# Performance work log

Hardware: AMD Instinct MI355X
Metric: run time of the kernel (lower is better)

The kernel has to match this reference:

```python
import jax, jax.numpy as jnp
import numpy as np

N = 10000          # nodes
E = 80000          # edges
STATE_DIM = 18
HID = 1024
LAYERS = 4


def setup_inputs() -> dict:
    key = jax.random.key(0)
    ks = jax.random.split(key, 16)
    s = 0.02
    x = jax.random.normal(ks[0], (N, STATE_DIM), dtype=jnp.float32)
    edge_index = jax.random.randint(ks[1], (2, E), 0, N, dtype=jnp.int32)
    # frozen inverse-phase embedding projection (no bias)
    proj_w = jax.random.normal(ks[2], (STATE_DIM, HID), dtype=jnp.float32) * s
    # per-layer message MLP: Linear(2*HID -> HID) -> ReLU -> Linear(HID -> HID)
    W1 = jax.random.normal(ks[3], (LAYERS, 2 * HID, HID), dtype=jnp.float32) * s
    b1 = jnp.zeros((LAYERS, HID), dtype=jnp.float32)
    W2 = jax.random.normal(ks[4], (LAYERS, HID, HID), dtype=jnp.float32) * s
    b2 = jnp.zeros((LAYERS, HID), dtype=jnp.float32)
    # ghost head: Linear(HID->256) -> ReLU -> Linear(256->1) -> Sigmoid
    gw1 = jax.random.normal(ks[5], (HID, 256), dtype=jnp.float32) * s
    gb1 = jnp.zeros((256,), dtype=jnp.float32)
    gw2 = jax.random.normal(ks[6], (256, 1), dtype=jnp.float32) * s
    gb2 = jnp.zeros((1,), dtype=jnp.float32)
    # state head: Linear(HID -> STATE_DIM)
    sw = jax.random.normal(ks[7], (HID, STATE_DIM), dtype=jnp.float32) * s
    sb = jnp.zeros((STATE_DIM,), dtype=jnp.float32)
    return {"x": x, "edge_index": edge_index, "proj_w": proj_w,
            "W1": W1, "b1": b1, "W2": W2, "b2": b2,
            "gw1": gw1, "gb1": gb1, "gw2": gw2, "gb2": gb2,
            "sw": sw, "sb": sb}


def reference(x, edge_index, proj_w, W1, b1, W2, b2, gw1, gb1, gw2, gb2, sw, sb):
    src = edge_index[0]  # j (source)
    dst = edge_index[1]  # i (target), aggr='add' scatters into i
    # InversePhaseEmbedding: sin(h)*cos(h)
    p = x @ proj_w                      # [N, HID]
    h = jnp.sin(p) * jnp.cos(p)
    for l in range(LAYERS):
        x_i = h[dst]                    # [E, HID] gather target feats
        x_j = h[src]                    # [E, HID] gather source feats
        msg = jnp.concatenate([x_i, x_j - x_i], axis=-1)  # [E, 2*HID]
        m = jax.nn.relu(msg @ W1[l] + b1[l]) @ W2[l] + b2[l]  # [E, HID]
        h = jax.ops.segment_sum(m, dst, num_segments=N)       # scatter-add
        h = jax.nn.relu(h)
    ghost_score = jax.nn.sigmoid(jax.nn.relu(h @ gw1 + gb1) @ gw2 + gb2)  # [N,1]
    stable_state = h @ sw + sb                                            # [N,18]
    return ghost_score, stable_state, h
```

## Files before the change

kernel.cpp:

```cpp
#include <hip/hip_runtime.h>
#include <hip/hip_bf16.h>
#include <math.h>

#define NN 10000
#define EE 80000
#define SDIM 18
#define HID 1024
#define NLAYERS 4
#define GHID 256

typedef __bf16 bf16;
typedef __bf16 bf16x8 __attribute__((ext_vector_type(8)));
typedef __bf16 bf16x4 __attribute__((ext_vector_type(4)));
typedef float f32x4 __attribute__((ext_vector_type(4)));

#define AS1C(p) ((const __attribute__((address_space(1))) void*)(p))
#define AS3(p)  ((__attribute__((address_space(3))) void*)(p))

__global__ void zeroi_kernel(int* __restrict__ p, int n) {
    int i = blockIdx.x * 256 + threadIdx.x;
    if (i < n) p[i] = 0;
}

__global__ void count_kernel(const int* __restrict__ ei, int* __restrict__ cnt) {
    int e = blockIdx.x * 256 + threadIdx.x;
    if (e < EE) atomicAdd(&cnt[ei[EE + e]], 1);
}

__global__ __launch_bounds__(256) void scan_kernel(const int* __restrict__ cnt,
                                                   int* __restrict__ offs,
                                                   int* __restrict__ cursor,
                                                   float* __restrict__ degF) {
    const int CH = 40;
    __shared__ int partial[256];
    int t = threadIdx.x;
    int base = t * CH;
    int local[CH];
    int sum = 0;
#pragma unroll
    for (int i = 0; i < CH; ++i) {
        int idx = base + i;
        int v = (idx < NN) ? cnt[idx] : 0;
        local[i] = sum;
        sum += v;
    }
    partial[t] = sum;
    __syncthreads();
    for (int off = 1; off < 256; off <<= 1) {
        int v = (t >= off) ? partial[t - off] : 0;
        __syncthreads();
        partial[t] += v;
        __syncthreads();
    }
    int excl = (t == 0) ? 0 : partial[t - 1];
#pragma unroll
    for (int i = 0; i < CH; ++i) {
        int idx = base + i;
        if (idx < NN) {
            int o = excl + local[i];
            offs[idx] = o;
            cursor[idx] = o;
            degF[idx] = (float)cnt[idx];
        }
    }
    if (t == 255) offs[NN] = partial[255];
}

__global__ void scatter_kernel(const int* __restrict__ ei, int* __restrict__ cursor,
                               int* __restrict__ esrc) {
    int e = blockIdx.x * 256 + threadIdx.x;
    if (e < EE) {
        int dst = ei[EE + e];
        int pos = atomicAdd(&cursor[dst], 1);
        esrc[pos] = ei[e];
    }
}

__global__ __launch_bounds__(256) void tconvW1_kernel(const float* __restrict__ W1,
                                                      bf16* __restrict__ WT) {
    __shared__ float td[32][33];
    __shared__ float tb[32][33];
    const size_t H2 = (size_t)HID * HID;
    const float* s = W1 + (size_t)blockIdx.z * 2 * H2;
    bf16* d = WT + (size_t)blockIdx.z * 2 * H2;
    int bx = blockIdx.x * 32;
    int by = blockIdx.y * 32;
    int tx = threadIdx.x, ty = threadIdx.y;
#pragma unroll
    for (int r = 0; r < 4; ++r) {
        int row = by + ty + r * 8;
        float vt = s[(size_t)row * HID + bx + tx];
        float vb = s[H2 + (size_t)row * HID + bx + tx];
        td[ty + r * 8][tx] = vt - vb;
        tb[ty + r * 8][tx] = vb;
    }
    __syncthreads();
#pragma unroll
    for (int r = 0; r < 4; ++r) {
        int orow = bx + ty + r * 8;
        d[(size_t)orow * HID + by + tx] = (bf16)td[tx][ty + r * 8];
        d[(size_t)(HID + orow) * HID + by + tx] = (bf16)tb[tx][ty + r * 8];
    }
}

__global__ __launch_bounds__(256) void tconv_kernel(const float* __restrict__ src, long sstride,
                                                    bf16* __restrict__ dst, long dstride,
                                                    int M, int N) {
    __shared__ float t[32][33];
    const float* s = src + (size_t)blockIdx.z * sstride;
    bf16* d = dst + (size_t)blockIdx.z * dstride;
    int bx = blockIdx.x * 32;
    int by = blockIdx.y * 32;
    int tx = threadIdx.x, ty = threadIdx.y;
#pragma unroll
    for (int r = 0; r < 4; ++r) {
        int row = by + ty + r * 8;
        t[ty + r * 8][tx] = s[(size_t)row * N + bx + tx];
    }
    __syncthreads();
#pragma unroll
    for (int r = 0; r < 4; ++r) {
        int orow = bx + ty + r * 8;
        d[(size_t)orow * M + by + tx] = (bf16)t[tx][ty + r * 8];
    }
}

__global__ void swt_kernel(const float* __restrict__ sw, bf16* __restrict__ swt) {
    int i = blockIdx.x * 256 + threadIdx.x;
    int n = i >> 10, k = i & 1023;
    swt[i] = (bf16)(n < SDIM ? sw[k * SDIM + n] : 0.f);
}

__global__ void bias2_kernel(const float* __restrict__ b1, float* __restrict__ cb) {
    int i = blockIdx.x * 256 + threadIdx.x;
    int l = i >> 11, c = i & 2047;
    cb[i] = (c < HID) ? b1[l * HID + c] : 0.f;
}

__global__ __launch_bounds__(256) void proj_kernel(const float* __restrict__ x,
                                                   const float* __restrict__ pw,
                                                   bf16* __restrict__ hb) {
    int row = blockIdx.y;
    int col = blockIdx.x * 256 + threadIdx.x;
    __shared__ float xr[SDIM];
    if (threadIdx.x < SDIM) xr[threadIdx.x] = x[row * SDIM + threadIdx.x];
    __syncthreads();
    float acc = 0.f;
#pragma unroll
    for (int k = 0; k < SDIM; ++k) acc += xr[k] * pw[k * HID + col];
    hb[(size_t)row * HID + col] = (bf16)(sinf(acc) * cosf(acc));
}

template <int RELU, int HAS_BIAS, int HAS_RS, int WF32, int WB16>
__global__ __launch_bounds__(256) void mgemm_kernel(const bf16* __restrict__ A,
                                                    const bf16* __restrict__ Bt,
                                                    float* __restrict__ C,
                                                    bf16* __restrict__ Cb,
                                                    const float* __restrict__ bias,
                                                    const float* __restrict__ rowscale,
                                                    int M, int N, int K) {
    __shared__ bf16 As[2 * 128 * 32];
    __shared__ bf16 Bs[2 * 128 * 32];
    const int tid = threadIdx.x;

    const int num_n = gridDim.x, num_m = gridDim.y;
    int bid = blockIdx.x + blockIdx.y * num_n;
    const int GROUP = 8;
    int width = GROUP * num_n;
    int group = bid / width;
    int rem = bid - group * width;
    int rows_ing = num_m - group * GROUP;
    rows_ing = rows_ing < GROUP ? rows_ing : GROUP;
    int by = group * GROUP + rem % rows_ing;
    int bx = rem / rows_ing;
    const int m0 = by * 128;
    const int n0 = bx * 128;

    const int wave = tid >> 6;
    const int wr = (wave >> 1) * 64, wc = (wave & 1) * 64;
    const int lane = tid & 63;
    const int quad = lane >> 4, r15 = lane & 15;

    f32x4 acc[4][4] = {};

    const int s0 = tid, s1 = 256 + tid;
    int ar0 = m0 + (s0 >> 2); ar0 = ar0 < M ? ar0 : M - 1;
    int ar1 = m0 + (s1 >> 2); ar1 = ar1 < M ? ar1 : M - 1;
    const bf16* ga0 = A + (size_t)ar0 * K + (s0 & 3) * 8;
    const bf16* ga1 = A + (size_t)ar1 * K + (s1 & 3) * 8;
    const bf16* gb0 = Bt + (size_t)(n0 + (s0 >> 2)) * K + (s0 & 3) * 8;
    const bf16* gb1 = Bt + (size_t)(n0 + (s1 >> 2)) * K + (s1 & 3) * 8;
    bf16* lA0 = As + (size_t)(tid & ~63) * 8;
    bf16* lA1 = As + (size_t)(256 + (tid & ~63)) * 8;
    bf16* lB0 = Bs + (size_t)(tid & ~63) * 8;
    bf16* lB1 = Bs + (size_t)(256 + (tid & ~63)) * 8;

    for (int k0 = 0; k0 < K; k0 += 64) {
        __syncthreads();
        __builtin_amdgcn_global_load_lds(AS1C(ga0 + k0), AS3(lA0), 16, 0, 0);
        __builtin_amdgcn_global_load_lds(AS1C(ga1 + k0), AS3(lA1), 16, 0, 0);
        __builtin_amdgcn_global_load_lds(AS1C(ga0 + k0 + 32), AS3(lA0 + 4096), 16, 0, 0);
        __builtin_amdgcn_global_load_lds(AS1C(ga1 + k0 + 32), AS3(lA1 + 4096), 16, 0, 0);
        __builtin_amdgcn_global_load_lds(AS1C(gb0 + k0), AS3(lB0), 16, 0, 0);
        __builtin_amdgcn_global_load_lds(AS1C(gb1 + k0), AS3(lB1), 16, 0, 0);
        __builtin_amdgcn_global_load_lds(AS1C(gb0 + k0 + 32), AS3(lB0 + 4096), 16, 0, 0);
        __builtin_amdgcn_global_load_lds(AS1C(gb1 + k0 + 32), AS3(lB1 + 4096), 16, 0, 0);
        __syncthreads();
#pragma unroll
        for (int hf = 0; hf < 2; ++hf) {
            bf16x8 af[4], bfr[4];
#pragma unroll
            for (int i = 0; i < 4; ++i)
                af[i] = *(const bf16x8*)(As + hf * 4096 + (wr + i * 16 + r15) * 32 + quad * 8);
#pragma unroll
            for (int j = 0; j < 4; ++j)
                bfr[j] = *(const bf16x8*)(Bs + hf * 4096 + (wc + j * 16 + r15) * 32 + quad * 8);
#pragma unroll
            for (int i = 0; i < 4; ++i)
#pragma unroll
                for (int j = 0; j < 4; ++j)
                    acc[i][j] = __builtin_amdgcn_mfma_f32_16x16x32_bf16(af[i], bfr[j], acc[i][j], 0, 0, 0);
        }
    }

#pragma unroll
    for (int i = 0; i < 4; ++i) {
#pragma unroll
        for (int r = 0; r < 4; ++r) {
            int grow = m0 + wr + i * 16 + quad * 4 + r;
            if (grow >= M) continue;
            float rs = HAS_RS ? rowscale[grow] : 1.f;
#pragma unroll
            for (int j = 0; j < 4; ++j) {
                int gcol = n0 + wc + j * 16 + r15;
                float v = acc[i][j][r];
                if (HAS_BIAS) v += rs * bias[gcol];
                if (RELU) v = fmaxf(v, 0.f);
                if (WF32) C[(size_t)grow * N + gcol] = v;
                if (WB16) Cb[(size_t)grow * N + gcol] = (bf16)v;
            }
        }
    }
}

__global__ __launch_bounds__(256) void gather_kernel(const int* __restrict__ offs,
                                                     const int* __restrict__ esrc,
                                                     const bf16* __restrict__ CB,
                                                     bf16* __restrict__ Sb) {
    int node = blockIdx.x;
    int c = threadIdx.x * 4;
    int k0 = offs[node], k1 = offs[node + 1];
    bf16x4 cv = *(const bf16x4*)(CB + (size_t)node * 2048 + c);
    float cx = (float)cv.x, cy = (float)cv.y, cz = (float)cv.z, cw = (float)cv.w;
    float ax = 0.f, ay = 0.f, az = 0.f, aw = 0.f;
    for (int k = k0; k < k1; ++k) {
        int s = esrc[k];
        bf16x4 bv = *(const bf16x4*)(CB + (size_t)s * 2048 + 1024 + c);
        ax += fmaxf(cx + (float)bv.x, 0.f);
        ay += fmaxf(cy + (float)bv.y, 0.f);
        az += fmaxf(cz + (float)bv.z, 0.f);
        aw += fmaxf(cw + (float)bv.w, 0.f);
    }
    bf16x4 o;
    o.x = (bf16)ax; o.y = (bf16)ay; o.z = (bf16)az; o.w = (bf16)aw;
    *(bf16x4*)(Sb + (size_t)node * HID + c) = o;
}

__global__ __launch_bounds__(64) void stable_mfma_kernel(const bf16* __restrict__ hb,
                                                         const bf16* __restrict__ swt,
                                                         const float* __restrict__ sb,
                                                         float* __restrict__ out) {
    int m0 = blockIdx.x * 16;
    int lane = threadIdx.x;
    int quad = lane >> 4, r15 = lane & 15;
    f32x4 acc0 = {}, acc1 = {};
    const bf16* arow = hb + (size_t)(m0 + r15) * HID + quad * 8;
    const bf16* b0 = swt + (size_t)r15 * HID + quad * 8;
    const bf16* b1p = swt + (size_t)(16 + r15) * HID + quad * 8;
    for (int k0 = 0; k0 < HID; k0 += 32) {
        bf16x8 af = *(const bf16x8*)(arow + k0);
        bf16x8 bf0 = *(const bf16x8*)(b0 + k0);
        bf16x8 bf1 = *(const bf16x8*)(b1p + k0);
        acc0 = __builtin_amdgcn_mfma_f32_16x16x32_bf16(af, bf0, acc0, 0, 0, 0);
        acc1 = __builtin_amdgcn_mfma_f32_16x16x32_bf16(af, bf1, acc1, 0, 0, 0);
    }
#pragma unroll
    for (int r = 0; r < 4; ++r) {
        int grow = m0 + quad * 4 + r;
        out[(size_t)grow * SDIM + r15] = acc0[r] + sb[r15];
        if (r15 < 2) out[(size_t)grow * SDIM + 16 + r15] = acc1[r] + sb[16 + r15];
    }
}

__global__ __launch_bounds__(256) void ghost_kernel(const float* __restrict__ g1,
                                                    const float* __restrict__ gw2,
                                                    const float* __restrict__ gb2,
                                                    float* __restrict__ out) {
    int row = blockIdx.x;
    int t = threadIdx.x;
    float v = g1[(size_t)row * GHID + t] * gw2[t];
#pragma unroll
    for (int o = 32; o > 0; o >>= 1) v += __shfl_down(v, o, 64);
    __shared__ float red[4];
    if ((t & 63) == 0) red[t >> 6] = v;
    __syncthreads();
    if (t == 0) {
        float s = red[0] + red[1] + red[2] + red[3] + gb2[0];
        out[row] = 1.f / (1.f + expf(-s));
    }
}

extern "C" void kernel_launch(void* const* d_in, const int* in_sizes, int n_in,
                              void* d_out, int out_size, void* d_ws, size_t ws_size,
                              hipStream_t stream) {
    const float* x   = (const float*)d_in[0];
    const int*   ei  = (const int*)d_in[1];
    const float* pw  = (const float*)d_in[2];
    const float* W1  = (const float*)d_in[3];
    const float* b1  = (const float*)d_in[4];
    const float* W2  = (const float*)d_in[5];
    const float* b2  = (const float*)d_in[6];
    const float* gw1 = (const float*)d_in[7];
    const float* gb1 = (const float*)d_in[8];
    const float* gw2 = (const float*)d_in[9];
    const float* gb2 = (const float*)d_in[10];
    const float* sw  = (const float*)d_in[11];
    const float* sb  = (const float*)d_in[12];

    float* out    = (float*)d_out;
    float* ghost  = out;
    float* stable = out + NN;
    float* h      = out + NN + NN * SDIM;

    const size_t H2 = (size_t)HID * HID;
    float* ws   = (float*)d_ws;
    float* g1   = ws;
    float* degF = g1 + (size_t)NN * GHID;
    float* cb   = degF + NN;
    bf16* hb    = (bf16*)(cb + 4 * 2048);
    bf16* Sb    = hb + (size_t)NN * HID;
    bf16* CB    = Sb + (size_t)NN * HID;
    bf16* WT    = CB + (size_t)NN * 2048;
    bf16* W2t   = WT + 8 * H2;
    bf16* gw1t  = W2t + 4 * H2;
    bf16* swt   = gw1t + (size_t)GHID * HID;
    int*  cnt    = (int*)(swt + 32 * 1024);
    int*  offs   = cnt + NN;
    int*  cursor = offs + NN + 1;
    int*  esrc   = cursor + NN;

    zeroi_kernel<<<dim3((NN + 255) / 256), 256, 0, stream>>>(cnt, NN);
    count_kernel<<<dim3((EE + 255) / 256), 256, 0, stream>>>(ei, cnt);
    scan_kernel<<<dim3(1), 256, 0, stream>>>(cnt, offs, cursor, degF);
    scatter_kernel<<<dim3((EE + 255) / 256), 256, 0, stream>>>(ei, cursor, esrc);

    dim3 tb(32, 8);
    tconvW1_kernel<<<dim3(32, 32, 4), tb, 0, stream>>>(W1, WT);
    tconv_kernel<<<dim3(32, 32, 4), tb, 0, stream>>>(W2, (long)H2, W2t, (long)H2, HID, HID);
    tconv_kernel<<<dim3(GHID / 32, HID / 32, 1), tb, 0, stream>>>(gw1, 0, gw1t, 0, HID, GHID);
    swt_kernel<<<dim3(32 * 1024 / 256), 256, 0, stream>>>(sw, swt);
    bias2_kernel<<<dim3(4 * 2048 / 256), 256, 0, stream>>>(b1, cb);

    proj_kernel<<<dim3(HID / 256, NN), 256, 0, stream>>>(x, pw, hb);

    dim3 gfused(2048 / 128, (NN + 127) / 128);
    dim3 gw2g(HID / 128, (NN + 127) / 128);
    for (int l = 0; l < NLAYERS; ++l) {
        mgemm_kernel<0, 1, 0, 0, 1><<<gfused, 256, 0, stream>>>(
            hb, WT + (size_t)l * 2 * H2, nullptr, CB, cb + l * 2048, nullptr, NN, 2048, HID);
        gather_kernel<<<dim3(NN), 256, 0, stream>>>(offs, esrc, CB, Sb);
        if (l < NLAYERS - 1)
            mgemm_kernel<1, 1, 1, 0, 1><<<gw2g, 256, 0, stream>>>(
                Sb, W2t + (size_t)l * H2, nullptr, hb, b2 + (size_t)l * HID, degF, NN, HID, HID);
        else
            mgemm_kernel<1, 1, 1, 1, 1><<<gw2g, 256, 0, stream>>>(
                Sb, W2t + (size_t)l * H2, h, hb, b2 + (size_t)l * HID, degF, NN, HID, HID);
    }

    mgemm_kernel<1, 1, 0, 1, 0><<<dim3(GHID / 128, (NN + 127) / 128), 256, 0, stream>>>(
        hb, gw1t, g1, nullptr, gb1, nullptr, NN, GHID, HID);
    ghost_kernel<<<dim3(NN), 256, 0, stream>>>(g1, gw2, gb2, ghost);
    stable_mfma_kernel<<<dim3(NN / 16), 64, 0, stream>>>(hb, swt, sb, stable);
}
```

Baseline: 777.3 us.

## Double-buffer GEMM LDS loads, merge prep kernels, widen gather and ghost kernels

The GEMM main loop now uses two LDS buffers with K-step 32, so the next tile is prefetched while MFMAs run on the current one. The earlier version loaded a 64-wide K slice under two barriers with no overlap. All weight transpose, bias and zeroing kernels are merged into one prep launch to cut launch overhead. The gather kernel handles two nodes per block with 8-wide bf16 vectors, and the ghost head uses one wave per row without shared-memory reduction. Risks are twice as many barriers per K and more LDS pressure in the GEMM.

Measured after the change: 750.8 us. 3.4% less time.

```diff
diff --git a/kernel.cpp b/kernel.cpp
--- a/kernel.cpp
+++ b/kernel.cpp
@@ -16,11 +16,6 @@
 
 #define AS1C(p) ((const __attribute__((address_space(1))) void*)(p))
 #define AS3(p)  ((__attribute__((address_space(3))) void*)(p))
-
-__global__ void zeroi_kernel(int* __restrict__ p, int n) {
-    int i = blockIdx.x * 256 + threadIdx.x;
-    if (i < n) p[i] = 0;
-}
 
 __global__ void count_kernel(const int* __restrict__ ei, int* __restrict__ cnt) {
     int e = blockIdx.x * 256 + threadIdx.x;
@@ -76,65 +71,86 @@
     }
 }
 
-__global__ __launch_bounds__(256) void tconvW1_kernel(const float* __restrict__ W1,
-                                                      bf16* __restrict__ WT) {
+__global__ __launch_bounds__(256) void prep_kernel(const float* __restrict__ W1,
+                                                   const float* __restrict__ W2,
+                                                   const float* __restrict__ gw1,
+                                                   const float* __restrict__ sw,
+                                                   const float* __restrict__ b1,
+                                                   bf16* __restrict__ WT,
+                                                   bf16* __restrict__ W2t,
+                                                   bf16* __restrict__ gw1t,
+                                                   bf16* __restrict__ swt,
+                                                   float* __restrict__ cb,
+                                                   int* __restrict__ cnt) {
     __shared__ float td[32][33];
     __shared__ float tb[32][33];
     const size_t H2 = (size_t)HID * HID;
-    const float* s = W1 + (size_t)blockIdx.z * 2 * H2;
-    bf16* d = WT + (size_t)blockIdx.z * 2 * H2;
-    int bx = blockIdx.x * 32;
-    int by = blockIdx.y * 32;
-    int tx = threadIdx.x, ty = threadIdx.y;
-#pragma unroll
-    for (int r = 0; r < 4; ++r) {
-        int row = by + ty + r * 8;
-        float vt = s[(size_t)row * HID + bx + tx];
-        float vb = s[H2 + (size_t)row * HID + bx + tx];
-        td[ty + r * 8][tx] = vt - vb;
-        tb[ty + r * 8][tx] = vb;
-    }
-    __syncthreads();
-#pragma unroll
-    for (int r = 0; r < 4; ++r) {
-        int orow = bx + ty + r * 8;
-        d[(size_t)orow * HID + by + tx] = (bf16)td[tx][ty + r * 8];
-        d[(size_t)(HID + orow) * HID + by + tx] = (bf16)tb[tx][ty + r * 8];
-    }
-}
-
-__global__ __launch_bounds__(256) void tconv_kernel(const float* __restrict__ src, long sstride,
-                                                    bf16* __restrict__ dst, long dstride,
-                                                    int M, int N) {
-    __shared__ float t[32][33];
-    const float* s = src + (size_t)blockIdx.z * sstride;
-    bf16* d = dst + (size_t)blockIdx.z * dstride;
-    int bx = blockIdx.x * 32;
-    int by = blockIdx.y * 32;
-    int tx = threadIdx.x, ty = threadIdx.y;
-#pragma unroll
-    for (int r = 0; r < 4; ++r) {
-        int row = by + ty + r * 8;
-        t[ty + r * 8][tx] = s[(size_t)row * N + bx + tx];
-    }
-    __syncthreads();
-#pragma unroll
-    for (int r = 0; r < 4; ++r) {
-        int orow = bx + ty + r * 8;
-        d[(size_t)orow * M + by + tx] = (bf16)t[tx][ty + r * 8];
-    }
-}
-
-__global__ void swt_kernel(const float* __restrict__ sw, bf16* __restrict__ swt) {
-    int i = blockIdx.x * 256 + threadIdx.x;
-    int n = i >> 10, k = i & 1023;
-    swt[i] = (bf16)(n < SDIM ? sw[k * SDIM + n] : 0.f);
-}
-
-__global__ void bias2_kernel(const float* __restrict__ b1, float* __restrict__ cb) {
-    int i = blockIdx.x * 256 + threadIdx.x;
-    int l = i >> 11, c = i & 2047;
-    cb[i] = (c < HID) ? b1[l * HID + c] : 0.f;
+    int b = blockIdx.x;
+    int tx = threadIdx.x & 31, ty = threadIdx.x >> 5;
+
+    if (b < 4096) {
+        int l = b >> 10, r = b & 1023;
+        int bx = (r & 31) * 32, by = (r >> 5) * 32;
+        const float* s = W1 + (size_t)l * 2 * H2;
+        bf16* d = WT + (size_t)l * 2 * H2;
+#pragma unroll
+        for (int r4 = 0; r4 < 4; ++r4) {
+            int row = by + ty + r4 * 8;
+            float vt = s[(size_t)row * HID + bx + tx];
+            float vb = s[H2 + (size_t)row * HID + bx + tx];
+            td[ty + r4 * 8][tx] = vt - vb;
+            tb[ty + r4 * 8][tx] = vb;
+        }
+        __syncthreads();
+#pragma unroll
+        for (int r4 = 0; r4 < 4; ++r4) {
+            int orow = bx + ty + r4 * 8;
+            d[(size_t)orow * HID + by + tx] = (bf16)td[tx][ty + r4 * 8];
+            d[(size_t)(HID + orow) * HID + by + tx] = (bf16)tb[tx][ty + r4 * 8];
+        }
+    } else if (b < 8192) {
+        int sub = b - 4096;
+        int l = sub >> 10, r = sub & 1023;
+        int bx = (r & 31) * 32, by = (r >> 5) * 32;
+        const float* s = W2 + (size_t)l * H2;
+        bf16* d = W2t + (size_t)l * H2;
+#pragma unroll
+        for (int r4 = 0; r4 < 4; ++r4) {
+            int row = by + ty + r4 * 8;
+            td[ty + r4 * 8][tx] = s[(size_t)row * HID + bx + tx];
+        }
+        __syncthreads();
+#pragma unroll
+        for (int r4 = 0; r4 < 4; ++r4) {
+            int orow = bx + ty + r4 * 8;
+            d[(size_t)orow * HID + by + tx] = (bf16)td[tx][ty + r4 * 8];
+        }
+    } else if (b < 8448) {
+        int sub = b - 8192;
+        int bx = (sub & 7) * 32, by = (sub >> 3) * 32;
+#pragma unroll
+        for (int r4 = 0; r4 < 4; ++r4) {
+            int row = by + ty + r4 * 8;
+            td[ty + r4 * 8][tx] = gw1[(size_t)row * GHID + bx + tx];
+        }
+        __syncthreads();
+#pragma unroll
+        for (int r4 = 0; r4 < 4; ++r4) {
+            int orow = bx + ty + r4 * 8;
+            gw1t[(size_t)orow * HID + by + tx] = (bf16)td[tx][ty + r4 * 8];
+        }
+    } else if (b < 8576) {
+        int i = (b - 8448) * 256 + threadIdx.x;
+        int n = i >> 10, k = i & 1023;
+        swt[i] = (bf16)(n < SDIM ? sw[k * SDIM + n] : 0.f);
+    } else if (b < 8608) {
+        int i = (b - 8576) * 256 + threadIdx.x;
+        int l = i >> 11, c = i & 2047;
+        cb[i] = (c < HID) ? b1[l * HID + c] : 0.f;
+    } else {
+        int i = (b - 8608) * 256 + threadIdx.x;
+        if (i < NN) cnt[i] = 0;
+    }
 }
 
 __global__ __launch_bounds__(256) void proj_kernel(const float* __restrict__ x,
@@ -159,8 +175,8 @@
                                                     const float* __restrict__ bias,
                                                     const float* __restrict__ rowscale,
                                                     int M, int N, int K) {
-    __shared__ bf16 As[2 * 128 * 32];
-    __shared__ bf16 Bs[2 * 128 * 32];
+    __shared__ bf16 As[2][128 * 32];
+    __shared__ bf16 Bs[2][128 * 32];
     const int tid = threadIdx.x;
 
     const int num_n = gridDim.x, num_m = gridDim.y;
@@ -190,37 +206,37 @@
     const bf16* ga1 = A + (size_t)ar1 * K + (s1 & 3) * 8;
     const bf16* gb0 = Bt + (size_t)(n0 + (s0 >> 2)) * K + (s0 & 3) * 8;
     const bf16* gb1 = Bt + (size_t)(n0 + (s1 >> 2)) * K + (s1 & 3) * 8;
-    bf16* lA0 = As + (size_t)(tid & ~63) * 8;
-    bf16* lA1 = As + (size_t)(256 + (tid & ~63)) * 8;
-    bf16* lB0 = Bs + (size_t)(tid & ~63) * 8;
-    bf16* lB1 = Bs + (size_t)(256 + (tid & ~63)) * 8;
-
-    for (int k0 = 0; k0 < K; k0 += 64) {
-        __syncthreads();
-        __builtin_amdgcn_global_load_lds(AS1C(ga0 + k0), AS3(lA0), 16, 0, 0);
-        __builtin_amdgcn_global_load_lds(AS1C(ga1 + k0), AS3(lA1), 16, 0, 0);
-        __builtin_amdgcn_global_load_lds(AS1C(ga0 + k0 + 32), AS3(lA0 + 4096), 16, 0, 0);
-        __builtin_amdgcn_global_load_lds(AS1C(ga1 + k0 + 32), AS3(lA1 + 4096), 16, 0, 0);
-        __builtin_amdgcn_global_load_lds(AS1C(gb0 + k0), AS3(lB0), 16, 0, 0);
-        __builtin_amdgcn_global_load_lds(AS1C(gb1 + k0), AS3(lB1), 16, 0, 0);
-        __builtin_amdgcn_global_load_lds(AS1C(gb0 + k0 + 32), AS3(lB0 + 4096), 16, 0, 0);
-        __builtin_amdgcn_global_load_lds(AS1C(gb1 + k0 + 32), AS3(lB1 + 4096), 16, 0, 0);
-        __syncthreads();
-#pragma unroll
-        for (int hf = 0; hf < 2; ++hf) {
-            bf16x8 af[4], bfr[4];
-#pragma unroll
-            for (int i = 0; i < 4; ++i)
-                af[i] = *(const bf16x8*)(As + hf * 4096 + (wr + i * 16 + r15) * 32 + quad * 8);
+    const int lofs0 = (tid & ~63) * 8;
+    const int lofs1 = 2048 + (tid & ~63) * 8;
+
+    __builtin_amdgcn_global_load_lds(AS1C(ga0), AS3(&As[0][lofs0]), 16, 0, 0);
+    __builtin_amdgcn_global_load_lds(AS1C(ga1), AS3(&As[0][lofs1]), 16, 0, 0);
+    __builtin_amdgcn_global_load_lds(AS1C(gb0), AS3(&Bs[0][lofs0]), 16, 0, 0);
+    __builtin_amdgcn_global_load_lds(AS1C(gb1), AS3(&Bs[0][lofs1]), 16, 0, 0);
+
+    const int NIT = K >> 5;
+    for (int k = 0; k < NIT; ++k) {
+        const int buf = k & 1;
+        __syncthreads();
+        if (k + 1 < NIT) {
+            const int ko = (k + 1) << 5;
+            __builtin_amdgcn_global_load_lds(AS1C(ga0 + ko), AS3(&As[buf ^ 1][lofs0]), 16, 0, 0);
+            __builtin_amdgcn_global_load_lds(AS1C(ga1 + ko), AS3(&As[buf ^ 1][lofs1]), 16, 0, 0);
+            __builtin_amdgcn_global_load_lds(AS1C(gb0 + ko), AS3(&Bs[buf ^ 1][lofs0]), 16, 0, 0);
+            __builtin_amdgcn_global_load_lds(AS1C(gb1 + ko), AS3(&Bs[buf ^ 1][lofs1]), 16, 0, 0);
+        }
+        bf16x8 af[4], bfr[4];
+#pragma unroll
+        for (int i = 0; i < 4; ++i)
+            af[i] = *(const bf16x8*)(&As[buf][(wr + i * 16 + r15) * 32 + quad * 8]);
+#pragma unroll
+        for (int j = 0; j < 4; ++j)
+            bfr[j] = *(const bf16x8*)(&Bs[buf][(wc + j * 16 + r15) * 32 + quad * 8]);
+#pragma unroll
+        for (int i = 0; i < 4; ++i)
 #pragma unroll
             for (int j = 0; j < 4; ++j)
-                bfr[j] = *(const bf16x8*)(Bs + hf * 4096 + (wc + j * 16 + r15) * 32 + quad * 8);
-#pragma unroll
-            for (int i = 0; i < 4; ++i)
-#pragma unroll
-                for (int j = 0; j < 4; ++j)
-                    acc[i][j] = __builtin_amdgcn_mfma_f32_16x16x32_bf16(af[i], bfr[j], acc[i][j], 0, 0, 0);
-        }
+                acc[i][j] = __builtin_amdgcn_mfma_f32_16x16x32_bf16(af[i], bfr[j], acc[i][j], 0, 0, 0);
     }
 
 #pragma unroll
@@ -247,23 +263,25 @@
                                                      const int* __restrict__ esrc,
                                                      const bf16* __restrict__ CB,
                                                      bf16* __restrict__ Sb) {
-    int node = blockIdx.x;
-    int c = threadIdx.x * 4;
+    int half = threadIdx.x >> 7;
+    int t = threadIdx.x & 127;
+    int node = blockIdx.x * 2 + half;
+    int c = t * 8;
     int k0 = offs[node], k1 = offs[node + 1];
-    bf16x4 cv = *(const bf16x4*)(CB + (size_t)node * 2048 + c);
-    float cx = (float)cv.x, cy = (float)cv.y, cz = (float)cv.z, cw = (float)cv.w;
-    float ax = 0.f, ay = 0.f, az = 0.f, aw = 0.f;
+    bf16x8 cv = *(const bf16x8*)(CB + (size_t)node * 2048 + c);
+    float cf[8], a[8];
+#pragma unroll
+    for (int i = 0; i < 8; ++i) { cf[i] = (float)cv[i]; a[i] = 0.f; }
     for (int k = k0; k < k1; ++k) {
         int s = esrc[k];
-        bf16x4 bv = *(const bf16x4*)(CB + (size_t)s * 2048 + 1024 + c);
-        ax += fmaxf(cx + (float)bv.x, 0.f);
-        ay += fmaxf(cy + (float)bv.y, 0.f);
-        az += fmaxf(cz + (float)bv.z, 0.f);
-        aw += fmaxf(cw + (float)bv.w, 0.f);
-    }
-    bf16x4 o;
-    o.x = (bf16)ax; o.y = (bf16)ay; o.z = (bf16)az; o.w = (bf16)aw;
-    *(bf16x4*)(Sb + (size_t)node * HID + c) = o;
+        bf16x8 bv = *(const bf16x8*)(CB + (size_t)s * 2048 + 1024 + c);
+#pragma unroll
+        for (int i = 0; i < 8; ++i) a[i] += fmaxf(cf[i] + (float)bv[i], 0.f);
+    }
+    bf16x8 o;
+#pragma unroll
+    for (int i = 0; i < 8; ++i) o[i] = (bf16)a[i];
+    *(bf16x8*)(Sb + (size_t)node * HID + c) = o;
 }
 
 __global__ __launch_bounds__(64) void stable_mfma_kernel(const bf16* __restrict__ hb,
@@ -296,18 +314,14 @@
                                                     const float* __restrict__ gw2,
                                                     const float* __restrict__ gb2,
                                                     float* __restrict__ out) {
-    int row = blockIdx.x;
-    int t = threadIdx.x;
-    float v = g1[(size_t)row * GHID + t] * gw2[t];
+    int w = threadIdx.x >> 6, lane = threadIdx.x & 63;
+    int row = blockIdx.x * 4 + w;
+    const float4 gv = *(const float4*)(g1 + (size_t)row * GHID + lane * 4);
+    const float4 wv = *(const float4*)(gw2 + lane * 4);
+    float v = gv.x * wv.x + gv.y * wv.y + gv.z * wv.z + gv.w * wv.w;
 #pragma unroll
     for (int o = 32; o > 0; o >>= 1) v += __shfl_down(v, o, 64);
-    __shared__ float red[4];
-    if ((t & 63) == 0) red[t >> 6] = v;
-    __syncthreads();
-    if (t == 0) {
-        float s = red[0] + red[1] + red[2] + red[3] + gb2[0];
-        out[row] = 1.f / (1.f + expf(-s));
-    }
+    if (lane == 0) out[row] = 1.f / (1.f + expf(-(v + gb2[0])));
 }
 
 extern "C" void kernel_launch(void* const* d_in, const int* in_sizes, int n_in,
@@ -349,17 +363,11 @@
     int*  cursor = offs + NN + 1;
     int*  esrc   = cursor + NN;
 
-    zeroi_kernel<<<dim3((NN + 255) / 256), 256, 0, stream>>>(cnt, NN);
+    prep_kernel<<<dim3(8648), 256, 0, stream>>>(W1, W2, gw1, sw, b1, WT, W2t, gw1t, swt, cb, cnt);
+
     count_kernel<<<dim3((EE + 255) / 256), 256, 0, stream>>>(ei, cnt);
     scan_kernel<<<dim3(1), 256, 0, stream>>>(cnt, offs, cursor, degF);
     scatter_kernel<<<dim3((EE + 255) / 256), 256, 0, stream>>>(ei, cursor, esrc);
-
-    dim3 tb(32, 8);
-    tconvW1_kernel<<<dim3(32, 32, 4), tb, 0, stream>>>(W1, WT);
-    tconv_kernel<<<dim3(32, 32, 4), tb, 0, stream>>>(W2, (long)H2, W2t, (long)H2, HID, HID);
-    tconv_kernel<<<dim3(GHID / 32, HID / 32, 1), tb, 0, stream>>>(gw1, 0, gw1t, 0, HID, GHID);
-    swt_kernel<<<dim3(32 * 1024 / 256), 256, 0, stream>>>(sw, swt);
-    bias2_kernel<<<dim3(4 * 2048 / 256), 256, 0, stream>>>(b1, cb);
 
     proj_kernel<<<dim3(HID / 256, NN), 256, 0, stream>>>(x, pw, hb);
 
@@ -368,7 +376,7 @@
     for (int l = 0; l < NLAYERS; ++l) {
         mgemm_kernel<0, 1, 0, 0, 1><<<gfused, 256, 0, stream>>>(
             hb, WT + (size_t)l * 2 * H2, nullptr, CB, cb + l * 2048, nullptr, NN, 2048, HID);
-        gather_kernel<<<dim3(NN), 256, 0, stream>>>(offs, esrc, CB, Sb);
+        gather_kernel<<<dim3(NN / 2), 256, 0, stream>>>(offs, esrc, CB, Sb);
         if (l < NLAYERS - 1)
             mgemm_kernel<1, 1, 1, 0, 1><<<gw2g, 256, 0, stream>>>(
                 Sb, W2t + (size_t)l * H2, nullptr, hb, b2 + (size_t)l * HID, degF, NN, HID, HID);
@@ -379,6 +387,6 @@
 
     mgemm_kernel<1, 1, 0, 1, 0><<<dim3(GHID / 128, (NN + 127) / 128), 256, 0, stream>>>(
         hb, gw1t, g1, nullptr, gb1, nullptr, NN, GHID, HID);
-    ghost_kernel<<<dim3(NN), 256, 0, stream>>>(g1, gw2, gb2, ghost);
+    ghost_kernel<<<dim3(NN / 4), 256, 0, stream>>>(g1, gw2, gb2, ghost);
     stable_mfma_kernel<<<dim3(NN / 16), 64, 0, stream>>>(hb, swt, sb, stable);
 }
```
